# Optimization experiments

Hardware: AMD Instinct MI355X
Metric: run time of the kernel (lower is better)

Reference implementation:

```python
import jax, jax.numpy as jnp
import numpy as np

N, NF, D, GH, E, B = 4096, 128, 64, 64, 32768, 32
NG, STEPS = 3, 3  # n_gcn, set2set processing steps


def setup_inputs() -> dict:
    key = jax.random.key(0)
    ks = iter(jax.random.split(key, 64))
    nrm = lambda shape: jax.random.normal(next(ks), shape, dtype=jnp.float32) * 0.05
    inp = {
        'x': jax.random.normal(next(ks), (N, NF), dtype=jnp.float32),
        'edge_attr': jax.random.uniform(next(ks), (E,), dtype=jnp.float32),
        'edge_idx': jax.random.randint(next(ks), (2, E), 0, N),
        'batch_map': jnp.sort(jax.random.randint(next(ks), (N,), 0, B)),
        # pre-GC MLP: NF->D, D->D, D->D (ReLU each)
        'pre_W0': nrm((NF, D)), 'pre_b0': nrm((D,)),
        'pre_W1': nrm((D, D)), 'pre_b1': nrm((D,)),
        'pre_W2': nrm((D, D)), 'pre_b2': nrm((D,)),
        # NNConv edge nets (stacked over NG layers): 1->GH->D*D
        'enn_W1': nrm((NG, 1, GH)), 'enn_b1': nrm((NG, GH)),
        'enn_W2': nrm((NG, GH, D * D)), 'enn_b2': nrm((NG, D * D)),
        'root_W': nrm((NG, D, D)), 'conv_b': nrm((NG, D)),
        # GRU(D, D) per layer, gate order r,z,n (torch), stored transposed for x@W
        'gru_Wih': nrm((NG, D, 3 * D)), 'gru_Whh': nrm((NG, D, 3 * D)),
        'gru_bih': nrm((NG, 3 * D)), 'gru_bhh': nrm((NG, 3 * D)),
        # Set2Set LSTM: input 2D -> hidden D, gate order i,f,g,o (torch)
        's2s_Wih': nrm((2 * D, 4 * D)), 's2s_Whh': nrm((D, 4 * D)),
        's2s_bih': nrm((4 * D,)), 's2s_bhh': nrm((4 * D,)),
        # post-GC MLP: 2D->D, D->D, D->D (ReLU each), then D->1
        'post_W0': nrm((2 * D, D)), 'post_b0': nrm((D,)),
        'post_W1': nrm((D, D)), 'post_b1': nrm((D,)),
        'post_W2': nrm((D, D)), 'post_b2': nrm((D,)),
        'post_W3': nrm((D, 1)), 'post_b3': nrm((1,)),
    }
    return inp


def _forward(x, edge_attr, pre_W0, pre_b0, pre_W1, pre_b1, pre_W2, pre_b2,
             enn_W1, enn_b1, enn_W2, enn_b2, root_W, conv_b,
             gru_Wih, gru_Whh, gru_bih, gru_bhh,
             s2s_Wih, s2s_Whh, s2s_bih, s2s_bhh,
             post_W0, post_b0, post_W1, post_b1, post_W2, post_b2,
             post_W3, post_b3, edge_idx, batch_map):
    relu, sig = jax.nn.relu, jax.nn.sigmoid
    # pre-GC layers
    out = relu(x @ pre_W0 + pre_b0)
    out = relu(out @ pre_W1 + pre_b1)
    out = relu(out @ pre_W2 + pre_b2)  # [N, D]

    src, dst = edge_idx[0], edge_idx[1]
    deg = jax.ops.segment_sum(jnp.ones((E,), out.dtype), dst, num_segments=N)
    deg = jnp.maximum(deg, 1.0)
    ea = edge_attr[:, None]  # view(-1, 1)

    for l in range(NG):
        h = out
        # NNConv: per-edge weight matrix from edge MLP
        We = relu(ea @ enn_W1[l] + enn_b1[l])              # [E, GH]
        We = (We @ enn_W2[l] + enn_b2[l]).reshape(E, D, D)  # [E, D, D]
        msg = jnp.einsum('ei,eio->eo', out[src], We)        # [E, D]
        agg = jax.ops.segment_sum(msg, dst, num_segments=N) / deg[:, None]
        conv = relu(agg + out @ root_W[l] + conv_b[l])
        # single-step GRU update (torch gate order r, z, n)
        gi = conv @ gru_Wih[l] + gru_bih[l]
        gh = h @ gru_Whh[l] + gru_bhh[l]
        i_r, i_z, i_n = jnp.split(gi, 3, axis=-1)
        h_r, h_z, h_n = jnp.split(gh, 3, axis=-1)
        r = sig(i_r + h_r)
        z = sig(i_z + h_z)
        n = jnp.tanh(i_n + r * h_n)
        out = (1.0 - z) * n + z * h

    # Set2Set pooling (early)
    q_star = jnp.zeros((B, 2 * D), out.dtype)
    hh = jnp.zeros((B, D), out.dtype)
    cc = jnp.zeros((B, D), out.dtype)
    for _ in range(STEPS):
        gates = q_star @ s2s_Wih + s2s_bih + hh @ s2s_Whh + s2s_bhh
        gi_, gf, gg, go = jnp.split(gates, 4, axis=-1)
        cc = sig(gf) * cc + sig(gi_) * jnp.tanh(gg)
        hh = sig(go) * jnp.tanh(cc)
        q = hh
        e = jnp.sum(out * q[batch_map], axis=-1)                    # [N]
        m = jax.ops.segment_max(e, batch_map, num_segments=B)
        a = jnp.exp(e - m[batch_map])
        den = jax.ops.segment_sum(a, batch_map, num_segments=B)
        a = a / den[batch_map]
        r_read = jax.ops.segment_sum(a[:, None] * out, batch_map, num_segments=B)
        q_star = jnp.concatenate([q, r_read], axis=-1)              # [B, 2D]

    # post-GC layers
    y = relu(q_star @ post_W0 + post_b0)
    y = relu(y @ post_W1 + post_b1)
    y = relu(y @ post_W2 + post_b2)
    y = y @ post_W3 + post_b3  # [B, 1]
    return y


def reference(x, edge_attr, edge_idx, batch_map, pre_W0, pre_b0, pre_W1, pre_b1,
              pre_W2, pre_b2, enn_W1, enn_b1, enn_W2, enn_b2, root_W, conv_b,
              gru_Wih, gru_Whh, gru_bih, gru_bhh, s2s_Wih, s2s_Whh, s2s_bih,
              s2s_bhh, post_W0, post_b0, post_W1, post_b1, post_W2, post_b2,
              post_W3, post_b3):
    return _forward(x, edge_attr, pre_W0, pre_b0, pre_W1, pre_b1, pre_W2, pre_b2,
                    enn_W1, enn_b1, enn_W2, enn_b2, root_W, conv_b,
                    gru_Wih, gru_Whh, gru_bih, gru_bhh,
                    s2s_Wih, s2s_Whh, s2s_bih, s2s_bhh,
                    post_W0, post_b0, post_W1, post_b1, post_W2, post_b2,
                    post_W3, post_b3, edge_idx, batch_map)
```

## Files before the change

kernel.cpp:

```cpp
#include <hip/hip_runtime.h>
#include <hip/hip_bf16.h>
#include <string.h>

#define NN   4096
#define NE   32768
#define NB   32
#define BKT  64
#define MSG_CHUNK 16

typedef __attribute__((ext_vector_type(8))) short short8;
typedef __attribute__((ext_vector_type(4))) float f4;

__device__ __forceinline__ float sigf(float x) { return 1.0f / (1.0f + __expf(-x)); }
__device__ __forceinline__ short f2bf(float f) {
    __hip_bfloat16 h = __float2bfloat16(f);
    short s;
    memcpy(&s, &h, sizeof(short));
    return s;
}

__global__ __launch_bounds__(256) void k_setup(const float* __restrict__ x,
        const float* __restrict__ W0, const float* __restrict__ b0,
        const float* __restrict__ W1, const float* __restrict__ b1,
        const float* __restrict__ W2, const float* __restrict__ b2,
        const float* __restrict__ enn_W2, __hip_bfloat16* __restrict__ W2F,
        float* __restrict__ out, float* __restrict__ agg,
        int* cnt_src, int* cnt_dst, int* bstart, int* bend) {
    int bid = blockIdx.x, t = threadIdx.x;
    if (bid < 32) {
        int i = bid * 256 + t;
        if (i < NN) cnt_src[i] = 0;
        else cnt_dst[i - NN] = 0;
        if (i < NB) { bstart[i] = 0x7FFFFFFF; bend[i] = 0; }
    } else if (bid < 224) {
        __shared__ __hip_bfloat16 tile[4096];
        size_t base = (size_t)(bid - 32) * 4096;
        for (int i = t; i < 4096; i += 256) {
            int k = i >> 6, o = i & 63;
            int pos = ((o >> 4) << 10) | ((k >> 5) << 9) | (((k >> 3) & 3) << 7)
                    | ((o & 15) << 3) | (k & 7);
            tile[pos] = __float2bfloat16(enn_W2[base + i]);
        }
        __syncthreads();
        for (int i = t; i < 4096; i += 256) W2F[base + i] = tile[i];
    } else {
        __shared__ float xr[4][128], ha[4][64], hb[4][64];
        int w = t >> 6, j = t & 63;
        int n = (bid - 224) * 4 + w;
        xr[w][j] = x[(size_t)n * 128 + j];
        xr[w][64 + j] = x[(size_t)n * 128 + 64 + j];
        agg[(size_t)n * 64 + j] = 0.f;
        float s = b0[j];
        #pragma unroll 8
        for (int k = 0; k < 128; ++k) s = fmaf(xr[w][k], W0[k * 64 + j], s);
        ha[w][j] = fmaxf(s, 0.f);
        s = b1[j];
        #pragma unroll 8
        for (int k = 0; k < 64; ++k) s = fmaf(ha[w][k], W1[k * 64 + j], s);
        hb[w][j] = fmaxf(s, 0.f);
        s = b2[j];
        #pragma unroll 8
        for (int k = 0; k < 64; ++k) s = fmaf(hb[w][k], W2[k * 64 + j], s);
        out[(size_t)n * 64 + j] = fmaxf(s, 0.f);
    }
}

__global__ __launch_bounds__(256) void k_bucket(const int* __restrict__ eidx,
        const float* __restrict__ ea, const int* __restrict__ bm,
        int* cnt_src, int* cnt_dst, int* csr_dst, float* csr_ea,
        int* bstart, int* bend) {
    int e = blockIdx.x * 256 + threadIdx.x;
    if (e < NE) {
        int s = eidx[e];
        int d = eidx[NE + e];
        int slot = atomicAdd(&cnt_src[s], 1);
        if (slot < BKT) {
            csr_dst[s * BKT + slot] = d;
            csr_ea[s * BKT + slot] = ea[e];
        }
        atomicAdd(&cnt_dst[d], 1);
    }
    if (e < NN) {
        int b = bm[e];
        atomicMin(&bstart[b], e);
        atomicMax(&bend[b], e + 1);
    }
}

__global__ __launch_bounds__(256, 1) void k_fused(const float* __restrict__ out,
        const __hip_bfloat16* __restrict__ W2F_l, const float* __restrict__ b2l,
        const float* __restrict__ W1l, const float* __restrict__ b1l,
        const int* __restrict__ cnt_src, const int* __restrict__ csr_dst,
        const float* __restrict__ csr_ea, float* __restrict__ agg) {
    __shared__ __hip_bfloat16 Pt[16 * 4096];
    __shared__ float outs[16][68];
    __shared__ float wlds[4][MSG_CHUNK][64];
    int t = threadIdx.x, wave = t >> 6, lane = t & 63;
    int laneM = lane & 15, quad = lane >> 4;
    int n0 = blockIdx.x * 16;
    for (int i = t; i < 1024; i += 256) outs[i >> 6][i & 63] = out[(size_t)n0 * 64 + i];
    __syncthreads();
    short8 a0, a1;
    {
        const float* ar = &outs[laneM][quad * 8];
        #pragma unroll
        for (int j = 0; j < 8; ++j) a0[j] = f2bf(ar[j]);
        const float* ar2 = &outs[laneM][32 + quad * 8];
        #pragma unroll
        for (int j = 0; j < 8; ++j) a1[j] = f2bf(ar2[j]);
    }
    float btr[4] = {0.f, 0.f, 0.f, 0.f};
    for (int k = 0; k < 64; ++k) {
        float bv = b2l[k * 64 + lane];
        #pragma unroll
        for (int u = 0; u < 4; ++u) btr[u] = fmaf(outs[wave * 4 + u][k], bv, btr[u]);
    }
    #pragma unroll 2
    for (int gp = 0; gp < 8; ++gp) {
        int g0 = wave * 16 + gp * 2;
        const __hip_bfloat16* BgA = W2F_l + (size_t)g0 * 4096;
        const __hip_bfloat16* BgB = BgA + 4096;
        int c = g0 >> 3, d = gp & 3;
        char* wb = (char*)Pt + (quad << 15) + (c << 10) + (laneM << 4)
                 + (((d ^ quad) & 3) << 2);
        #pragma unroll
        for (int sub = 0; sub < 4; ++sub) {
            short8 bA0 = *(const short8*)(BgA + sub * 1024 + lane * 8);
            short8 bA1 = *(const short8*)(BgA + sub * 1024 + 512 + lane * 8);
            short8 bB0 = *(const short8*)(BgB + sub * 1024 + lane * 8);
            short8 bB1 = *(const short8*)(BgB + sub * 1024 + 512 + lane * 8);
            f4 accA = {0.f, 0.f, 0.f, 0.f}, accB = {0.f, 0.f, 0.f, 0.f};
            accA = __builtin_amdgcn_mfma_f32_16x16x32_bf16(a0, bA0, accA, 0, 0, 0);
            accA = __builtin_amdgcn_mfma_f32_16x16x32_bf16(a1, bA1, accA, 0, 0, 0);
            accB = __builtin_amdgcn_mfma_f32_16x16x32_bf16(a0, bB0, accB, 0, 0, 0);
            accB = __builtin_amdgcn_mfma_f32_16x16x32_bf16(a1, bB1, accB, 0, 0, 0);
            char* wbs = wb + (sub << 8);
            #pragma unroll
            for (int r = 0; r < 4; ++r) {
                unsigned pk = (unsigned)(unsigned short)f2bf(accA[r])
                            | ((unsigned)(unsigned short)f2bf(accB[r]) << 16);
                *(unsigned*)(wbs + (r << 13)) = pk;
            }
        }
    }
    __syncthreads();
    float w1v = W1l[lane], b1v = b1l[lane];
    for (int u = 0; u < 4; ++u) {
        int nloc = wave * 4 + u;
        int n = n0 + nloc;
        int deg = cnt_src[n];
        if (deg > BKT) deg = BKT;
        if (deg <= 0) continue;
        float preg[64];
        const char* Pn = (const char*)Pt + (nloc << 13);
        #pragma unroll
        for (int c = 0; c < 8; ++c) {
            uint4 vv = *(const uint4*)(Pn + (c << 10) + (lane << 4));
            unsigned d0 = vv.x, d1 = vv.y, d2 = vv.z, d3 = vv.w;
            if (wave & 1) { unsigned tt = d0; d0 = d1; d1 = tt; tt = d2; d2 = d3; d3 = tt; }
            if (wave & 2) { unsigned tt = d0; d0 = d2; d2 = tt; tt = d1; d1 = d3; d3 = tt; }
            union { unsigned u2; float f; } cv;
            cv.u2 = d0 << 16;          preg[c * 8 + 0] = cv.f;
            cv.u2 = d0 & 0xFFFF0000u;  preg[c * 8 + 1] = cv.f;
            cv.u2 = d1 << 16;          preg[c * 8 + 2] = cv.f;
            cv.u2 = d1 & 0xFFFF0000u;  preg[c * 8 + 3] = cv.f;
            cv.u2 = d2 << 16;          preg[c * 8 + 4] = cv.f;
            cv.u2 = d2 & 0xFFFF0000u;  preg[c * 8 + 5] = cv.f;
            cv.u2 = d3 << 16;          preg[c * 8 + 6] = cv.f;
            cv.u2 = d3 & 0xFFFF0000u;  preg[c * 8 + 7] = cv.f;
        }
        float bt = btr[u];
        const int* bdst = csr_dst + n * BKT;
        const float* bea = csr_ea + n * BKT;
        for (int c0 = 0; c0 < deg; c0 += MSG_CHUNK) {
            int cc = deg - c0;
            if (cc > MSG_CHUNK) cc = MSG_CHUNK;
            int dl = 0; float el = 0.f;
            if (lane < cc) { dl = bdst[c0 + lane]; el = bea[c0 + lane]; }
            for (int si = 0; si < cc; ++si) {
                float eav = __shfl(el, si, 64);
                wlds[wave][si][lane] = fmaxf(fmaf(eav, w1v, b1v), 0.f);
            }
            for (int i = 0; i < cc; ++i) {
                int dst = __shfl(dl, i, 64);
                const float* wr = wlds[wave][i];
                float acc0 = bt, acc1 = 0.f, acc2 = 0.f, acc3 = 0.f;
                #pragma unroll
                for (int g = 0; g < 64; g += 16) {
                    float4 w0 = *(const float4*)(wr + g);
                    float4 w1 = *(const float4*)(wr + g + 4);
                    float4 w2 = *(const float4*)(wr + g + 8);
                    float4 w3 = *(const float4*)(wr + g + 12);
                    acc0 = fmaf(w0.x, preg[g], acc0);
                    acc0 = fmaf(w0.y, preg[g + 1], acc0);
                    acc0 = fmaf(w0.z, preg[g + 2], acc0);
                    acc0 = fmaf(w0.w, preg[g + 3], acc0);
                    acc1 = fmaf(w1.x, preg[g + 4], acc1);
                    acc1 = fmaf(w1.y, preg[g + 5], acc1);
                    acc1 = fmaf(w1.z, preg[g + 6], acc1);
                    acc1 = fmaf(w1.w, preg[g + 7], acc1);
                    acc2 = fmaf(w2.x, preg[g + 8], acc2);
                    acc2 = fmaf(w2.y, preg[g + 9], acc2);
                    acc2 = fmaf(w2.z, preg[g + 10], acc2);
                    acc2 = fmaf(w2.w, preg[g + 11], acc2);
                    acc3 = fmaf(w3.x, preg[g + 12], acc3);
                    acc3 = fmaf(w3.y, preg[g + 13], acc3);
                    acc3 = fmaf(w3.z, preg[g + 14], acc3);
                    acc3 = fmaf(w3.w, preg[g + 15], acc3);
                }
                float acc = (acc0 + acc1) + (acc2 + acc3);
                atomicAdd(&agg[(size_t)dst * 64 + lane], acc);
            }
        }
    }
}

__global__ __launch_bounds__(256) void k_gru(const float* __restrict__ out,
        float* __restrict__ agg, const int* __restrict__ cnt_dst,
        const float* __restrict__ rootW, const float* __restrict__ convb,
        const float* __restrict__ Wih, const float* __restrict__ Whh,
        const float* __restrict__ bih, const float* __restrict__ bhh,
        float* __restrict__ outn) {
    __shared__ float sh[4][64], sc[4][64];
    int t = threadIdx.x, w = t >> 6, j = t & 63;
    int n = blockIdx.x * 4 + w;
    float hj = out[(size_t)n * 64 + j];
    sh[w][j] = hj;
    int dg = cnt_dst[n];
    float invd = 1.0f / (float)(dg > 0 ? dg : 1);
    float av = agg[(size_t)n * 64 + j];
    agg[(size_t)n * 64 + j] = 0.f;
    __syncthreads();
    float s = av * invd + convb[j];
    #pragma unroll 8
    for (int k = 0; k < 64; ++k) s = fmaf(sh[w][k], rootW[k * 64 + j], s);
    float conv = fmaxf(s, 0.f);
    sc[w][j] = conv;
    __syncthreads();
    float gir = bih[j], giz = bih[64 + j], gin = bih[128 + j];
    float ghr = bhh[j], ghz = bhh[64 + j], ghn = bhh[128 + j];
    #pragma unroll 4
    for (int k = 0; k < 64; ++k) {
        float c = sc[w][k], h = sh[w][k];
        gir = fmaf(c, Wih[k * 192 + j], gir);
        giz = fmaf(c, Wih[k * 192 + 64 + j], giz);
        gin = fmaf(c, Wih[k * 192 + 128 + j], gin);
        ghr = fmaf(h, Whh[k * 192 + j], ghr);
        ghz = fmaf(h, Whh[k * 192 + 64 + j], ghz);
        ghn = fmaf(h, Whh[k * 192 + 128 + j], ghn);
    }
    float r = sigf(gir + ghr);
    float z = sigf(giz + ghz);
    float nn = tanhf(gin + r * ghn);
    outn[(size_t)n * 64 + j] = (1.f - z) * nn + z * hj;
}

__global__ __launch_bounds__(1024) void k_s2s_post(const float* __restrict__ out,
        const int* __restrict__ bstart, const int* __restrict__ bend,
        const float* __restrict__ Wih, const float* __restrict__ Whh,
        const float* __restrict__ bih, const float* __restrict__ bhh,
        const float* __restrict__ pW0, const float* __restrict__ pb0,
        const float* __restrict__ pW1, const float* __restrict__ pb1,
        const float* __restrict__ pW2, const float* __restrict__ pb2,
        const float* __restrict__ pW3, const float* __restrict__ pb3,
        float* __restrict__ y) {
    __shared__ float cache[192 * 65];
    __shared__ float qs[128], hh[64], cc[64], gates[256];
    __shared__ float ebuf[1024];
    __shared__ float redbuf[1024];
    __shared__ float redw[16];
    __shared__ float smax, sinv;
    __shared__ float tmp64[64];
    int t = threadIdx.x, wave = t >> 6, lane = t & 63;
    int b = blockIdx.x;
    int s0 = bstart[b], e0 = bend[b];
    int cnt = e0 - s0;
    if (cnt < 0) cnt = 0;
    if (cnt > 1024) cnt = 1024;
    int ccnt = cnt < 192 ? cnt : 192;
    for (int li = t; li < ccnt * 64; li += 1024) {
        int rowi = li >> 6, d = li & 63;
        cache[rowi * 65 + d] = out[(size_t)(s0 + rowi) * 64 + d];
    }
    int g = t & 255, seg = t >> 8;
    const float* wp;
    int kcnt;
    if (seg == 0)      { wp = Wih + g;             kcnt = 64; }
    else if (seg == 1) { wp = Wih + 64 * 256 + g;  kcnt = 64; }
    else if (seg == 2) { wp = Whh + g;             kcnt = 32; }
    else               { wp = Whh + 32 * 256 + g;  kcnt = 32; }
    float wreg[64];
    #pragma unroll
    for (int j = 0; j < 64; ++j)
        wreg[j] = (j < kcnt) ? wp[(size_t)j * 256] : 0.f;
    if (t < 128) qs[t] = 0.f;
    if (t < 64) { hh[t] = 0.f; cc[t] = 0.f; }
    __syncthreads();
    for (int step = 0; step < 3; ++step) {
        const float* vsrc = (seg == 0) ? qs : (seg == 1) ? qs + 64
                          : (seg == 2) ? hh : hh + 32;
        float partial = 0.f;
        #pragma unroll
        for (int j = 0; j < 64; ++j)
            if (j < kcnt) partial = fmaf(vsrc[j], wreg[j], partial);
        redbuf[seg * 256 + g] = partial;
        __syncthreads();
        if (t < 256)
            gates[t] = bih[t] + bhh[t] + redbuf[t] + redbuf[256 + t]
                     + redbuf[512 + t] + redbuf[768 + t];
        __syncthreads();
        if (t < 64) {
            float cn = sigf(gates[64 + t]) * cc[t] + sigf(gates[t]) * tanhf(gates[128 + t]);
            cc[t] = cn;
            hh[t] = sigf(gates[192 + t]) * tanhf(cn);
        }
        __syncthreads();
        for (int idx = t; idx < cnt; idx += 1024) {
            float s = 0.f;
            if (idx < 192) {
                const float* row = cache + idx * 65;
                #pragma unroll 8
                for (int d = 0; d < 64; ++d) s = fmaf(row[d], hh[d], s);
            } else {
                const float* row = out + (size_t)(s0 + idx) * 64;
                for (int d = 0; d < 64; ++d) s = fmaf(row[d], hh[d], s);
            }
            ebuf[idx] = s;
        }
        __syncthreads();
        float lm = (t < cnt) ? ebuf[t] : -3.0e38f;
        #pragma unroll
        for (int off = 32; off > 0; off >>= 1) lm = fmaxf(lm, __shfl_down(lm, off, 64));
        if (lane == 0) redw[wave] = lm;
        __syncthreads();
        if (t == 0) {
            float m = redw[0];
            #pragma unroll
            for (int w2 = 1; w2 < 16; ++w2) m = fmaxf(m, redw[w2]);
            smax = m;
        }
        __syncthreads();
        float m = smax;
        float av = 0.f;
        if (t < cnt) {
            av = __expf(ebuf[t] - m);
            ebuf[t] = av;
        }
        float ls = av;
        #pragma unroll
        for (int off = 32; off > 0; off >>= 1) ls += __shfl_down(ls, off, 64);
        if (lane == 0) redw[wave] = ls;
        __syncthreads();
        if (t == 0) {
            float s = 0.f;
            #pragma unroll
            for (int w2 = 0; w2 < 16; ++w2) s += redw[w2];
            sinv = (cnt > 0) ? 1.f / s : 0.f;
        }
        __syncthreads();
        float inv = sinv;
        float r = 0.f;
        for (int idx = wave; idx < cnt; idx += 16) {
            float a = ebuf[idx];
            float v = (idx < 192) ? cache[idx * 65 + lane]
                                  : out[(size_t)(s0 + idx) * 64 + lane];
            r = fmaf(a, v, r);
        }
        redbuf[wave * 64 + lane] = r;
        __syncthreads();
        if (t < 64) {
            float s = 0.f;
            #pragma unroll
            for (int w2 = 0; w2 < 16; ++w2) s += redbuf[w2 * 64 + t];
            qs[64 + t] = s * inv;
            qs[t] = hh[t];
        }
        __syncthreads();
    }
    if (t < 64) {
        float s = pb0[t];
        #pragma unroll 4
        for (int k = 0; k < 128; ++k) s = fmaf(qs[k], pW0[k * 64 + t], s);
        tmp64[t] = fmaxf(s, 0.f);
    }
    __syncthreads();
    float h1v = 0.f;
    if (t < 64) {
        float s = pb1[t];
        #pragma unroll 4
        for (int k = 0; k < 64; ++k) s = fmaf(tmp64[k], pW1[k * 64 + t], s);
        h1v = fmaxf(s, 0.f);
    }
    __syncthreads();
    if (t < 64) tmp64[t] = h1v;
    __syncthreads();
    if (t < 64) {
        float s = pb2[t];
        #pragma unroll 4
        for (int k = 0; k < 64; ++k) s = fmaf(tmp64[k], pW2[k * 64 + t], s);
        gates[t] = fmaxf(s, 0.f) * pW3[t];
    }
    __syncthreads();
    if (t == 0) {
        float yy = pb3[0];
        for (int k = 0; k < 64; ++k) yy += gates[k];
        y[b] = yy;
    }
}


extern "C" void kernel_launch(void* const* d_in, const int* in_sizes, int n_in,
                              void* d_out, int out_size, void* d_ws, size_t ws_size,
                              hipStream_t stream) {
    const float* x         = (const float*)d_in[0];
    const float* edge_attr = (const float*)d_in[1];
    const int*   edge_idx  = (const int*)d_in[2];
    const int*   batch_map = (const int*)d_in[3];
    const float* pre_W0 = (const float*)d_in[4];
    const float* pre_b0 = (const float*)d_in[5];
    const float* pre_W1 = (const float*)d_in[6];
    const float* pre_b1 = (const float*)d_in[7];
    const float* pre_W2 = (const float*)d_in[8];
    const float* pre_b2 = (const float*)d_in[9];
    const float* enn_W1 = (const float*)d_in[10];
    const float* enn_b1 = (const float*)d_in[11];
    const float* enn_W2 = (const float*)d_in[12];
    const float* enn_b2 = (const float*)d_in[13];
    const float* root_W = (const float*)d_in[14];
    const float* conv_b = (const float*)d_in[15];
    const float* gru_Wih = (const float*)d_in[16];
    const float* gru_Whh = (const float*)d_in[17];
    const float* gru_bih = (const float*)d_in[18];
    const float* gru_bhh = (const float*)d_in[19];
    const float* s2s_Wih = (const float*)d_in[20];
    const float* s2s_Whh = (const float*)d_in[21];
    const float* s2s_bih = (const float*)d_in[22];
    const float* s2s_bhh = (const float*)d_in[23];
    const float* post_W0 = (const float*)d_in[24];
    const float* post_b0 = (const float*)d_in[25];
    const float* post_W1 = (const float*)d_in[26];
    const float* post_b1 = (const float*)d_in[27];
    const float* post_W2 = (const float*)d_in[28];
    const float* post_b2 = (const float*)d_in[29];
    const float* post_W3 = (const float*)d_in[30];
    const float* post_b3 = (const float*)d_in[31];
    float* yout = (float*)d_out;

    char* wp = (char*)d_ws;
    auto take = [&](size_t bytes) -> char* {
        char* r = wp;
        wp += (bytes + 255) & ~(size_t)255;
        return r;
    };
    float* outA = (float*)take((size_t)NN * 64 * 4);
    float* outB = (float*)take((size_t)NN * 64 * 4);
    float* agg  = (float*)take((size_t)NN * 64 * 4);
    __hip_bfloat16* W2F = (__hip_bfloat16*)take((size_t)3 * 64 * 4096 * 2);
    int* cnt_src  = (int*)take((size_t)NN * 4);
    int* cnt_dst  = (int*)take((size_t)NN * 4);
    int* csr_dst  = (int*)take((size_t)NN * BKT * 4);
    float* csr_ea = (float*)take((size_t)NN * BKT * 4);
    int* bstart   = (int*)take((size_t)NB * 4);
    int* bend     = (int*)take((size_t)NB * 4);

    k_setup<<<1248, 256, 0, stream>>>(x, pre_W0, pre_b0, pre_W1, pre_b1, pre_W2, pre_b2,
                                      enn_W2, W2F, outA, agg, cnt_src, cnt_dst,
                                      bstart, bend);
    k_bucket<<<128, 256, 0, stream>>>(edge_idx, edge_attr, batch_map, cnt_src, cnt_dst,
                                      csr_dst, csr_ea, bstart, bend);

    float* cur = outA;
    float* nxt = outB;
    for (int l = 0; l < 3; ++l) {
        k_fused<<<NN / 16, 256, 0, stream>>>(cur, W2F + (size_t)l * 64 * 4096,
                                             enn_b2 + (size_t)l * 4096,
                                             enn_W1 + l * 64, enn_b1 + l * 64,
                                             cnt_src, csr_dst, csr_ea, agg);
        k_gru<<<NN / 4, 256, 0, stream>>>(cur, agg, cnt_dst, root_W + l * 4096,
                                          conv_b + l * 64, gru_Wih + l * 64 * 192,
                                          gru_Whh + l * 64 * 192, gru_bih + l * 192,
                                          gru_bhh + l * 192, nxt);
        float* tmp = cur; cur = nxt; nxt = tmp;
    }
    k_s2s_post<<<NB, 1024, 0, stream>>>(cur, bstart, bend, s2s_Wih, s2s_Whh, s2s_bih,
                                        s2s_bhh, post_W0, post_b0, post_W1, post_b1,
                                        post_W2, post_b2, post_W3, post_b3, yout);
}
```

Before: 372.1 us.

## Split NNConv message kernel over four hidden-channel chunks per node tile

The fused edge-message kernel now launches four blocks per 16-node tile, each computing the projection for only 16 of the 64 edge-net hidden channels. This shrinks shared memory from 128KB to 32KB and per-lane registers from 64 to 16 preg values, so launch bounds can request 3 blocks per CU. The aim is higher occupancy and more parallelism. The cost is four times as many atomicAdds to agg, since each chunk adds a partial sum, and the bias term is added only by chunk 0.

```diff
diff --git a/kernel.cpp b/kernel.cpp
--- a/kernel.cpp
+++ b/kernel.cpp
@@ -87,17 +87,18 @@
     }
 }
 
-__global__ __launch_bounds__(256, 1) void k_fused(const float* __restrict__ out,
+__global__ __launch_bounds__(256, 3) void k_fused(const float* __restrict__ out,
         const __hip_bfloat16* __restrict__ W2F_l, const float* __restrict__ b2l,
         const float* __restrict__ W1l, const float* __restrict__ b1l,
         const int* __restrict__ cnt_src, const int* __restrict__ csr_dst,
         const float* __restrict__ csr_ea, float* __restrict__ agg) {
-    __shared__ __hip_bfloat16 Pt[16 * 4096];
+    __shared__ __hip_bfloat16 Pt[16 * 16 * 64];
     __shared__ float outs[16][68];
-    __shared__ float wlds[4][MSG_CHUNK][64];
+    __shared__ float wlds[4][MSG_CHUNK][16];
     int t = threadIdx.x, wave = t >> 6, lane = t & 63;
     int laneM = lane & 15, quad = lane >> 4;
-    int n0 = blockIdx.x * 16;
+    int ntile = blockIdx.x >> 2, gc = blockIdx.x & 3;
+    int n0 = ntile * 16;
     for (int i = t; i < 1024; i += 256) outs[i >> 6][i & 63] = out[(size_t)n0 * 64 + i];
     __syncthreads();
     short8 a0, a1;
@@ -110,19 +111,23 @@
         for (int j = 0; j < 8; ++j) a1[j] = f2bf(ar2[j]);
     }
     float btr[4] = {0.f, 0.f, 0.f, 0.f};
-    for (int k = 0; k < 64; ++k) {
-        float bv = b2l[k * 64 + lane];
-        #pragma unroll
-        for (int u = 0; u < 4; ++u) btr[u] = fmaf(outs[wave * 4 + u][k], bv, btr[u]);
-    }
-    #pragma unroll 2
-    for (int gp = 0; gp < 8; ++gp) {
-        int g0 = wave * 16 + gp * 2;
-        const __hip_bfloat16* BgA = W2F_l + (size_t)g0 * 4096;
+    if (gc == 0) {
+        for (int k = 0; k < 64; ++k) {
+            float bv = b2l[k * 64 + lane];
+            #pragma unroll
+            for (int u = 0; u < 4; ++u) btr[u] = fmaf(outs[wave * 4 + u][k], bv, btr[u]);
+        }
+    }
+    #pragma unroll
+    for (int gp = 0; gp < 2; ++gp) {
+        int glA = wave * 4 + gp * 2;
+        int gA = gc * 16 + glA;
+        const __hip_bfloat16* BgA = W2F_l + (size_t)gA * 4096;
         const __hip_bfloat16* BgB = BgA + 4096;
-        int c = g0 >> 3, d = gp & 3;
-        char* wb = (char*)Pt + (quad << 15) + (c << 10) + (laneM << 4)
-                 + (((d ^ quad) & 3) << 2);
+        int half = glA >> 3;
+        int p = (glA >> 1) & 3;
+        char* wb = (char*)Pt + (quad << 13) + (half << 10) + (laneM << 4)
+                 + (((p ^ quad) & 3) << 2);
         #pragma unroll
         for (int sub = 0; sub < 4; ++sub) {
             short8 bA0 = *(const short8*)(BgA + sub * 1024 + lane * 8);
@@ -139,35 +144,35 @@
             for (int r = 0; r < 4; ++r) {
                 unsigned pk = (unsigned)(unsigned short)f2bf(accA[r])
                             | ((unsigned)(unsigned short)f2bf(accB[r]) << 16);
-                *(unsigned*)(wbs + (r << 13)) = pk;
+                *(unsigned*)(wbs + (r << 11)) = pk;
             }
         }
     }
     __syncthreads();
-    float w1v = W1l[lane], b1v = b1l[lane];
+    float w1v = W1l[gc * 16 + laneM], b1v = b1l[gc * 16 + laneM];
     for (int u = 0; u < 4; ++u) {
         int nloc = wave * 4 + u;
         int n = n0 + nloc;
         int deg = cnt_src[n];
         if (deg > BKT) deg = BKT;
         if (deg <= 0) continue;
-        float preg[64];
-        const char* Pn = (const char*)Pt + (nloc << 13);
-        #pragma unroll
-        for (int c = 0; c < 8; ++c) {
-            uint4 vv = *(const uint4*)(Pn + (c << 10) + (lane << 4));
+        float preg[16];
+        const char* Pn = (const char*)Pt + (nloc << 11);
+        #pragma unroll
+        for (int h = 0; h < 2; ++h) {
+            uint4 vv = *(const uint4*)(Pn + (h << 10) + (lane << 4));
             unsigned d0 = vv.x, d1 = vv.y, d2 = vv.z, d3 = vv.w;
             if (wave & 1) { unsigned tt = d0; d0 = d1; d1 = tt; tt = d2; d2 = d3; d3 = tt; }
             if (wave & 2) { unsigned tt = d0; d0 = d2; d2 = tt; tt = d1; d1 = d3; d3 = tt; }
             union { unsigned u2; float f; } cv;
-            cv.u2 = d0 << 16;          preg[c * 8 + 0] = cv.f;
-            cv.u2 = d0 & 0xFFFF0000u;  preg[c * 8 + 1] = cv.f;
-            cv.u2 = d1 << 16;          preg[c * 8 + 2] = cv.f;
-            cv.u2 = d1 & 0xFFFF0000u;  preg[c * 8 + 3] = cv.f;
-            cv.u2 = d2 << 16;          preg[c * 8 + 4] = cv.f;
-            cv.u2 = d2 & 0xFFFF0000u;  preg[c * 8 + 5] = cv.f;
-            cv.u2 = d3 << 16;          preg[c * 8 + 6] = cv.f;
-            cv.u2 = d3 & 0xFFFF0000u;  preg[c * 8 + 7] = cv.f;
+            cv.u2 = d0 << 16;          preg[h * 8 + 0] = cv.f;
+            cv.u2 = d0 & 0xFFFF0000u;  preg[h * 8 + 1] = cv.f;
+            cv.u2 = d1 << 16;          preg[h * 8 + 2] = cv.f;
+            cv.u2 = d1 & 0xFFFF0000u;  preg[h * 8 + 3] = cv.f;
+            cv.u2 = d2 << 16;          preg[h * 8 + 4] = cv.f;
+            cv.u2 = d2 & 0xFFFF0000u;  preg[h * 8 + 5] = cv.f;
+            cv.u2 = d3 << 16;          preg[h * 8 + 6] = cv.f;
+            cv.u2 = d3 & 0xFFFF0000u;  preg[h * 8 + 7] = cv.f;
         }
         float bt = btr[u];
         const int* bdst = csr_dst + n * BKT;
@@ -177,37 +182,35 @@
             if (cc > MSG_CHUNK) cc = MSG_CHUNK;
             int dl = 0; float el = 0.f;
             if (lane < cc) { dl = bdst[c0 + lane]; el = bea[c0 + lane]; }
-            for (int si = 0; si < cc; ++si) {
-                float eav = __shfl(el, si, 64);
-                wlds[wave][si][lane] = fmaxf(fmaf(eav, w1v, b1v), 0.f);
+            #pragma unroll
+            for (int j = 0; j < 4; ++j) {
+                float eav = __shfl(el, quad + 4 * j, 64);
+                wlds[wave][quad + 4 * j][laneM] = fmaxf(fmaf(eav, w1v, b1v), 0.f);
             }
             for (int i = 0; i < cc; ++i) {
                 int dst = __shfl(dl, i, 64);
                 const float* wr = wlds[wave][i];
+                float4 w0 = *(const float4*)(wr);
+                float4 w1 = *(const float4*)(wr + 4);
+                float4 w2 = *(const float4*)(wr + 8);
+                float4 w3 = *(const float4*)(wr + 12);
                 float acc0 = bt, acc1 = 0.f, acc2 = 0.f, acc3 = 0.f;
-                #pragma unroll
-                for (int g = 0; g < 64; g += 16) {
-                    float4 w0 = *(const float4*)(wr + g);
-                    float4 w1 = *(const float4*)(wr + g + 4);
-                    float4 w2 = *(const float4*)(wr + g + 8);
-                    float4 w3 = *(const float4*)(wr + g + 12);
-                    acc0 = fmaf(w0.x, preg[g], acc0);
-                    acc0 = fmaf(w0.y, preg[g + 1], acc0);
-                    acc0 = fmaf(w0.z, preg[g + 2], acc0);
-                    acc0 = fmaf(w0.w, preg[g + 3], acc0);
-                    acc1 = fmaf(w1.x, preg[g + 4], acc1);
-                    acc1 = fmaf(w1.y, preg[g + 5], acc1);
-                    acc1 = fmaf(w1.z, preg[g + 6], acc1);
-                    acc1 = fmaf(w1.w, preg[g + 7], acc1);
-                    acc2 = fmaf(w2.x, preg[g + 8], acc2);
-                    acc2 = fmaf(w2.y, preg[g + 9], acc2);
-                    acc2 = fmaf(w2.z, preg[g + 10], acc2);
-                    acc2 = fmaf(w2.w, preg[g + 11], acc2);
-                    acc3 = fmaf(w3.x, preg[g + 12], acc3);
-                    acc3 = fmaf(w3.y, preg[g + 13], acc3);
-                    acc3 = fmaf(w3.z, preg[g + 14], acc3);
-                    acc3 = fmaf(w3.w, preg[g + 15], acc3);
-                }
+                acc0 = fmaf(w0.x, preg[0], acc0);
+                acc0 = fmaf(w0.y, preg[1], acc0);
+                acc0 = fmaf(w0.z, preg[2], acc0);
+                acc0 = fmaf(w0.w, preg[3], acc0);
+                acc1 = fmaf(w1.x, preg[4], acc1);
+                acc1 = fmaf(w1.y, preg[5], acc1);
+                acc1 = fmaf(w1.z, preg[6], acc1);
+                acc1 = fmaf(w1.w, preg[7], acc1);
+                acc2 = fmaf(w2.x, preg[8], acc2);
+                acc2 = fmaf(w2.y, preg[9], acc2);
+                acc2 = fmaf(w2.z, preg[10], acc2);
+                acc2 = fmaf(w2.w, preg[11], acc2);
+                acc3 = fmaf(w3.x, preg[12], acc3);
+                acc3 = fmaf(w3.y, preg[13], acc3);
+                acc3 = fmaf(w3.z, preg[14], acc3);
+                acc3 = fmaf(w3.w, preg[15], acc3);
                 float acc = (acc0 + acc1) + (acc2 + acc3);
                 atomicAdd(&agg[(size_t)dst * 64 + lane], acc);
             }
@@ -472,10 +475,10 @@
     float* cur = outA;
     float* nxt = outB;
     for (int l = 0; l < 3; ++l) {
-        k_fused<<<NN / 16, 256, 0, stream>>>(cur, W2F + (size_t)l * 64 * 4096,
-                                             enn_b2 + (size_t)l * 4096,
-                                             enn_W1 + l * 64, enn_b1 + l * 64,
-                                             cnt_src, csr_dst, csr_ea, agg);
+        k_fused<<<NN / 16 * 4, 256, 0, stream>>>(cur, W2F + (size_t)l * 64 * 4096,
+                                                 enn_b2 + (size_t)l * 4096,
+                                                 enn_W1 + l * 64, enn_b1 + l * 64,
+                                                 cnt_src, csr_dst, csr_ea, agg);
         k_gru<<<NN / 4, 256, 0, stream>>>(cur, agg, cnt_dst, root_W + l * 4096,
                                           conv_b + l * 64, gru_Wih + l * 64 * 192,
                                           gru_Whh + l * 64 * 192, gru_bih + l * 192,
```

Result: no change. 378.3 us (+1.7%).
